# Kernel tuning notes

Measured on AMD Instinct MI355X. Metric: run time of the kernel, lower is better.

## Reference

```python
import jax, jax.numpy as jnp
import numpy as np

B, C, P, T = 16, 128, 512, 32
H = 2
D = C // H  # 64
SCALE = D ** -0.5  # note: original scales by d^-0.5, NOT (d*t)^-0.5


def setup_inputs() -> dict:
    key = jax.random.key(0)
    kx, kw, kb = jax.random.split(key, 3)
    x = jax.random.normal(kx, (B, C, P, T), dtype=jnp.float32)
    # Conv2d(C, 3C, kernel=1) == per-pixel linear: W:[3C, C], b:[3C]
    W = jax.random.normal(kw, (3 * C, C), dtype=jnp.float32) * (C ** -0.5)
    b = jax.random.normal(kb, (3 * C,), dtype=jnp.float32) * 0.01
    return {"x": x, "W": W, "b": b}


def reference(x, W, b):
    # 1x1 conv -> pointwise channel mix
    qkv = jnp.einsum('bcpt,oc->bopt', x, W) + b[None, :, None, None]  # [B,3C,P,T]
    qkv = qkv.reshape(B, 3, H, D, P, T)
    q, k, v = qkv[:, 0], qkv[:, 1], qkv[:, 2]  # each [B,H,D,P,T]
    # flatten (d t) as feature dim, tokens along P
    q = q.transpose(0, 1, 3, 2, 4).reshape(B, H, P, D * T)
    k = k.transpose(0, 1, 3, 2, 4).reshape(B, H, P, D * T)
    v = v.transpose(0, 1, 3, 2, 4).reshape(B, H, P, D * T)
    dots = jnp.einsum('bhpe,bhqe->bhpq', q, k) * SCALE  # [B,H,P,P]
    attn = jax.nn.softmax(dots, axis=-1)
    out = jnp.einsum('bhpq,bhqe->bhpe', attn, v)  # [B,H,P,D*T]
    # b h p (d t) -> b (h d) p t
    out = out.reshape(B, H, P, D, T).transpose(0, 1, 3, 2, 4).reshape(B, C, P, T)
    return out
```

## Files before the change

kernel.cpp:

```cpp
#include <hip/hip_runtime.h>

#define BB 16
#define CC 128
#define PP 512
#define TT 32
#define HH 2
#define DD 64
#define EE 2048
#define NPIX 16384
#define SCALE 0.125f

typedef _Float16 f16_t;
typedef _Float16 f16x8_t __attribute__((ext_vector_type(8)));
typedef _Float16 f16x4_t __attribute__((ext_vector_type(4)));
typedef float    f32x4_t __attribute__((ext_vector_type(4)));

#define AS_GLOBAL __attribute__((address_space(1)))
#define AS_LDS    __attribute__((address_space(3)))

__device__ __forceinline__ void async_ld16(const void* g, void* l) {
    __builtin_amdgcn_global_load_lds((const AS_GLOBAL void*)g,
                                     (AS_LDS void*)l, 16, 0, 0);
}

__device__ __forceinline__ void gemm_lds_bt(const f16_t* __restrict__ A, int lda,
                                            const f16_t* __restrict__ Bt, int ldb,
                                            int K, int m0, int n0,
                                            f16_t* As, f16_t* Bs,
                                            f32x4_t acc[4][4])
{
    const int tid  = threadIdx.x;
    const int lane = tid & 63;
    const int wave = tid >> 6;
    const int wm = wave & 1, wn = wave >> 1;
    const int quad = lane >> 4, l16 = lane & 15;

    const f16_t* gA0 = A  + (size_t)(m0 + lane)      * lda + wave * 8;
    const f16_t* gA1 = A  + (size_t)(m0 + 64 + lane) * lda + wave * 8;
    const f16_t* gB0 = Bt + (size_t)(n0 + lane)      * ldb + wave * 8;
    const f16_t* gB1 = Bt + (size_t)(n0 + 64 + lane) * ldb + wave * 8;
    f16_t* lA0 = As + (size_t)(wave * 128)      * 8;
    f16_t* lA1 = As + (size_t)(wave * 128 + 64) * 8;
    f16_t* lB0 = Bs + (size_t)(wave * 128)      * 8;
    f16_t* lB1 = Bs + (size_t)(wave * 128 + 64) * 8;

    const int ar = wm * 64 + l16;
    const int br = wn * 64 + l16;

    for (int k0 = 0; k0 < K; k0 += 32) {
        if (k0) __syncthreads();
        async_ld16(gA0 + k0, lA0);
        async_ld16(gA1 + k0, lA1);
        async_ld16(gB0 + k0, lB0);
        async_ld16(gB1 + k0, lB1);
        __syncthreads();

        f16x8_t af[4], bf[4];
#pragma unroll
        for (int mi = 0; mi < 4; ++mi)
            af[mi] = *(const f16x8_t*)(As + (size_t)(quad * 128 + ar + mi * 16) * 8);
#pragma unroll
        for (int ni = 0; ni < 4; ++ni)
            bf[ni] = *(const f16x8_t*)(Bs + (size_t)(quad * 128 + br + ni * 16) * 8);
#pragma unroll
        for (int mi = 0; mi < 4; ++mi)
#pragma unroll
            for (int ni = 0; ni < 4; ++ni)
                acc[mi][ni] = __builtin_amdgcn_mfma_f32_16x16x32_f16(
                    af[mi], bf[ni], acc[mi][ni], 0, 0, 0);
    }
}

__global__ __launch_bounds__(256) void wcvt_kernel(const float* __restrict__ W,
                                                   f16_t* __restrict__ Wh)
{
    const int i = (blockIdx.x * 256 + threadIdx.x) * 4;
    const float4 wv = *(const float4*)(W + i);
    f16x4_t t;
    t[0] = (_Float16)wv.x; t[1] = (_Float16)wv.y;
    t[2] = (_Float16)wv.z; t[3] = (_Float16)wv.w;
    *(f16x4_t*)(Wh + i) = t;
}

__global__ __launch_bounds__(256, 3) void proj_kernel(const float* __restrict__ x,
                                                      const f16_t* __restrict__ Wh,
                                                      const float* __restrict__ bias,
                                                      f16_t* __restrict__ q,
                                                      f16_t* __restrict__ k,
                                                      f16_t* __restrict__ v)
{
    __shared__ f16_t xs[CC * 128];
    __shared__ f16_t wbuf[8 * 128 * 8];
    const int b    = blockIdx.y;
    const int pt   = blockIdx.x;
    const int tid  = threadIdx.x;
    const int lane = tid & 63;
    const int wave = tid >> 6;
    const int wm   = wave & 1, wn = wave >> 1;
    const int quad = lane >> 4, l16 = lane & 15;
    const int pixb = pt * 128;

    const float* xb = x + (size_t)b * CC * NPIX;

#pragma unroll 2
    for (int r = 0; r < 8; ++r) {
        const int u  = r * 4 + wave;
        const int c0 = (u >> 1) * 8;
        const int pl = (u & 1) * 64 + lane;
        const float* g = xb + (size_t)c0 * NPIX + pixb + pl;
        float vv[8];
#pragma unroll
        for (int j = 0; j < 8; ++j) vv[j] = g[(size_t)j * NPIX];
        f16x8_t t;
#pragma unroll
        for (int j = 0; j < 8; ++j) t[j] = (_Float16)vv[j];
        *(f16x8_t*)((char*)xs + pl * 256 + ((c0 * 2) ^ ((pl & 15) << 4))) = t;
    }

    for (int s = 0; s < 3; ++s) {
        f32x4_t acc[4][4];
#pragma unroll
        for (int i = 0; i < 4; ++i)
#pragma unroll
            for (int j = 0; j < 4; ++j) acc[i][j] = (f32x4_t){0.f, 0.f, 0.f, 0.f};

#pragma unroll
        for (int khalf = 0; khalf < 2; ++khalf) {
            __syncthreads();
#pragma unroll
            for (int i = 0; i < 4; ++i) {
                const int idx = wave * 4 + i;
                const int ch  = idx >> 1;
                const int oh  = (idx & 1) * 64;
                async_ld16(Wh + (size_t)(s * 128 + oh + lane) * CC
                              + (khalf * 8 + ch) * 8,
                           wbuf + ((size_t)ch * 128 + oh) * 8);
            }
            __syncthreads();

#pragma unroll
            for (int kk = 0; kk < 2; ++kk) {
                const int k0  = khalf * 64 + kk * 32;
                const int kq  = k0 + quad * 8;
                const int chq = kk * 4 + quad;
                f16x8_t xf[4], wf[4];
#pragma unroll
                for (int mi = 0; mi < 4; ++mi) {
                    const int pl = wm * 64 + mi * 16 + l16;
                    xf[mi] = *(const f16x8_t*)((char*)xs + pl * 256 +
                                               ((kq * 2) ^ ((pl & 15) << 4)));
                }
#pragma unroll
                for (int ni = 0; ni < 4; ++ni) {
                    const int ol = wn * 64 + ni * 16 + l16;
                    wf[ni] = *(const f16x8_t*)(wbuf + ((size_t)chq * 128 + ol) * 8);
                }
#pragma unroll
                for (int mi = 0; mi < 4; ++mi)
#pragma unroll
                    for (int ni = 0; ni < 4; ++ni)
                        acc[mi][ni] = __builtin_amdgcn_mfma_f32_16x16x32_f16(
                            xf[mi], wf[ni], acc[mi][ni], 0, 0, 0);
            }
        }

        float bv[4];
#pragma unroll
        for (int ni = 0; ni < 4; ++ni)
            bv[ni] = bias[s * 128 + wn * 64 + ni * 16 + l16];

        f16_t* dst = (s == 0) ? q : (s == 1) ? k : v;
        const int h = wn;
#pragma unroll
        for (int mi = 0; mi < 4; ++mi) {
            const int pix0 = pixb + wm * 64 + mi * 16 + quad * 4;
            const int p  = pix0 >> 5;
            const int t0 = pix0 & 31;
#pragma unroll
            for (int ni = 0; ni < 4; ++ni) {
                const int d = ni * 16 + l16;
                f16x4_t o4;
#pragma unroll
                for (int r = 0; r < 4; ++r)
                    o4[r] = (_Float16)(acc[mi][ni][r] + bv[ni]);
                *(f16x4_t*)(dst + ((size_t)((b * HH + h) * PP + p)) * EE
                                + d * TT + t0) = o4;
            }
        }
    }
}

__global__ __launch_bounds__(256) void vpose_kernel(const f16_t* __restrict__ v,
                                                    f16_t* __restrict__ vt)
{
    __shared__ unsigned short lds[64][65];
    const int bh   = blockIdx.y;
    const int tile = blockIdx.x;
    const int e0 = (tile & 31) * 64;
    const int p0 = (tile >> 5) * 64;
    const int tid = threadIdx.x;
    const int rw  = tid >> 3;
    const int c8  = (tid & 7) * 8;
    const f16_t* vb  = v  + (size_t)bh * PP * EE;
    f16_t*       vtb = vt + (size_t)bh * EE * PP;
#pragma unroll
    for (int half = 0; half < 2; ++half) {
        const int p = rw + half * 32;
        const f16x8_t t = *(const f16x8_t*)(vb + (size_t)(p0 + p) * EE + e0 + c8);
#pragma unroll
        for (int j = 0; j < 8; ++j)
            lds[p][c8 + j] = __builtin_bit_cast(unsigned short, (_Float16)t[j]);
    }
    __syncthreads();
#pragma unroll
    for (int half = 0; half < 2; ++half) {
        const int e = rw + half * 32;
        f16x8_t t;
#pragma unroll
        for (int j = 0; j < 8; ++j)
            t[j] = __builtin_bit_cast(_Float16, lds[c8 + j][e]);
        *(f16x8_t*)(vtb + (size_t)(e0 + e) * PP + p0 + c8) = t;
    }
}

__global__ __launch_bounds__(256) void qk_kernel(const f16_t* __restrict__ q,
                                                 const f16_t* __restrict__ k,
                                                 float* __restrict__ S)
{
    __shared__ f16_t As[128 * 32];
    __shared__ f16_t Bs[128 * 32];
    const int id = blockIdx.x;
    const int bh = id & 31;
    const int tile = id >> 5;
    const int mt = tile & 3, nt = tile >> 2;
    const int tid  = threadIdx.x;
    const int lane = tid & 63;
    const int wave = tid >> 6;
    const int wm = wave & 1, wn = wave >> 1;
    const int quad = lane >> 4, l16 = lane & 15;

    f32x4_t acc[4][4];
#pragma unroll
    for (int i = 0; i < 4; ++i)
#pragma unroll
        for (int j = 0; j < 4; ++j) acc[i][j] = (f32x4_t){0.f, 0.f, 0.f, 0.f};

    const f16_t* qb = q + (size_t)bh * PP * EE;
    const f16_t* kb = k + (size_t)bh * PP * EE;
    gemm_lds_bt(qb, EE, kb, EE, EE, mt * 128, nt * 128, As, Bs, acc);

    float* Sb = S + (size_t)bh * PP * PP;
#pragma unroll
    for (int mi = 0; mi < 4; ++mi)
#pragma unroll
        for (int r = 0; r < 4; ++r) {
            const int row = mt * 128 + wm * 64 + mi * 16 + quad * 4 + r;
#pragma unroll
            for (int ni = 0; ni < 4; ++ni) {
                const int col = nt * 128 + wn * 64 + ni * 16 + l16;
                Sb[(size_t)row * PP + col] = acc[mi][ni][r] * SCALE;
            }
        }
}

__global__ __launch_bounds__(256) void softmax_kernel(float* __restrict__ S)
{
    const int tid  = threadIdx.x;
    const int wave = tid >> 6;
    const int lane = tid & 63;
    const int row  = blockIdx.x * 4 + wave;
    float* rp = S + (size_t)row * PP;

    const float4 a = *(const float4*)(rp + lane * 8);
    const float4 b = *(const float4*)(rp + lane * 8 + 4);

    float m = fmaxf(fmaxf(fmaxf(a.x, a.y), fmaxf(a.z, a.w)),
                    fmaxf(fmaxf(b.x, b.y), fmaxf(b.z, b.w)));
#pragma unroll
    for (int off = 1; off < 64; off <<= 1) m = fmaxf(m, __shfl_xor(m, off, 64));

    float e[8];
    e[0] = expf(a.x - m); e[1] = expf(a.y - m);
    e[2] = expf(a.z - m); e[3] = expf(a.w - m);
    e[4] = expf(b.x - m); e[5] = expf(b.y - m);
    e[6] = expf(b.z - m); e[7] = expf(b.w - m);

    float sum = e[0] + e[1] + e[2] + e[3] + e[4] + e[5] + e[6] + e[7];
#pragma unroll
    for (int off = 1; off < 64; off <<= 1) sum += __shfl_xor(sum, off, 64);
    const float inv = 1.0f / sum;

    __syncthreads();

    f16_t* prow = (f16_t*)rp;
    f16x8_t o;
#pragma unroll
    for (int j = 0; j < 8; ++j) o[j] = (_Float16)(e[j] * inv);
    *(f16x8_t*)(prow + lane * 8) = o;
}

__global__ __launch_bounds__(256) void pv_kernel(const f16_t* __restrict__ Pm,
                                                 const f16_t* __restrict__ vt,
                                                 float* __restrict__ out)
{
    __shared__ f16_t As[128 * 32];
    __shared__ f16_t Bs[128 * 32];
    const int id = blockIdx.x;
    const int bh = id & 31;
    const int tile = id >> 5;
    const int nt = tile & 3, mt = tile >> 2;
    const int tid  = threadIdx.x;
    const int lane = tid & 63;
    const int wave = tid >> 6;
    const int wm = wave & 1, wn = wave >> 1;
    const int quad = lane >> 4, l16 = lane & 15;

    f32x4_t acc[4][4];
#pragma unroll
    for (int i = 0; i < 4; ++i)
#pragma unroll
        for (int j = 0; j < 4; ++j) acc[i][j] = (f32x4_t){0.f, 0.f, 0.f, 0.f};

    const f16_t* Pb  = Pm + (size_t)bh * PP * 1024;
    const f16_t* vtb = vt + (size_t)bh * EE * PP;
    gemm_lds_bt(vtb, PP, Pb, 1024, PP, mt * 128, nt * 128, As, Bs, acc);

    const int b = bh >> 1, h = bh & 1;
#pragma unroll
    for (int mi = 0; mi < 4; ++mi) {
        const int e0 = mt * 128 + wm * 64 + mi * 16 + quad * 4;
        const int d  = e0 >> 5;
        const int t0 = e0 & 31;
#pragma unroll
        for (int ni = 0; ni < 4; ++ni) {
            const int p = nt * 128 + wn * 64 + ni * 16 + l16;
            *(f32x4_t*)(out + ((size_t)(b * CC + h * DD + d) * PP + p) * TT + t0)
                = acc[mi][ni];
        }
    }
}

extern "C" void kernel_launch(void* const* d_in, const int* in_sizes, int n_in,
                              void* d_out, int out_size, void* d_ws, size_t ws_size,
                              hipStream_t stream)
{
    const float* x    = (const float*)d_in[0];
    const float* W    = (const float*)d_in[1];
    const float* bias = (const float*)d_in[2];
    float* out = (float*)d_out;

    char* ws = (char*)d_ws;
    const size_t MiB = 1024ull * 1024ull;
    f16_t* q  = (f16_t*)(ws);
    f16_t* k  = (f16_t*)(ws + 64 * MiB);
    f16_t* v  = (f16_t*)(ws + 128 * MiB);
    f16_t* vt = (f16_t*)(ws + 192 * MiB);
    float* S  = (float*)(ws + 256 * MiB);
    f16_t* Wh = (f16_t*)(ws + 256 * MiB);

    wcvt_kernel<<<dim3(48), dim3(256), 0, stream>>>(W, Wh);
    proj_kernel<<<dim3(128, 16), dim3(256), 0, stream>>>(x, Wh, bias, q, k, v);
    vpose_kernel<<<dim3(256, 32), dim3(256), 0, stream>>>(v, vt);
    qk_kernel<<<dim3(512), dim3(256), 0, stream>>>(q, k, S);
    softmax_kernel<<<dim3(4096), dim3(256), 0, stream>>>(S);
    pv_kernel<<<dim3(2048), dim3(256), 0, stream>>>((const f16_t*)S, vt, out);
}
```

Before: 494.7 us.

## Double-buffer LDS tiles in QK and PV GEMMs to overlap loads with MFMA

Changes the shared GEMM loop so the next K-slice is loaded into a second LDS buffer with async global-to-LDS loads while MFMAs run on the current one. Explicit vmcnt waits and raw s_barrier calls replace the two __syncthreads per step. The goal is to hide global load latency in the QK and PV kernels. It doubles LDS per block to 32 KB, which can lower occupancy, and correctness depends on the hand-written waitcnt ordering.

```diff
diff --git a/kernel.cpp b/kernel.cpp
--- a/kernel.cpp
+++ b/kernel.cpp
@@ -23,51 +23,68 @@
                                      (AS_LDS void*)l, 16, 0, 0);
 }
 
-__device__ __forceinline__ void gemm_lds_bt(const f16_t* __restrict__ A, int lda,
-                                            const f16_t* __restrict__ Bt, int ldb,
-                                            int K, int m0, int n0,
-                                            f16_t* As, f16_t* Bs,
-                                            f32x4_t acc[4][4])
+__device__ __forceinline__ void gemm_lds_bt_pipe(const f16_t* __restrict__ A, int lda,
+                                                 const f16_t* __restrict__ Bt, int ldb,
+                                                 int K, int m0, int n0,
+                                                 f16_t* As, f16_t* Bs,
+                                                 f32x4_t acc[4][4])
 {
     const int tid  = threadIdx.x;
     const int lane = tid & 63;
     const int wave = tid >> 6;
     const int wm = wave & 1, wn = wave >> 1;
     const int quad = lane >> 4, l16 = lane & 15;
+    constexpr int TILE = 128 * 32;
 
     const f16_t* gA0 = A  + (size_t)(m0 + lane)      * lda + wave * 8;
     const f16_t* gA1 = A  + (size_t)(m0 + 64 + lane) * lda + wave * 8;
     const f16_t* gB0 = Bt + (size_t)(n0 + lane)      * ldb + wave * 8;
     const f16_t* gB1 = Bt + (size_t)(n0 + 64 + lane) * ldb + wave * 8;
-    f16_t* lA0 = As + (size_t)(wave * 128)      * 8;
-    f16_t* lA1 = As + (size_t)(wave * 128 + 64) * 8;
-    f16_t* lB0 = Bs + (size_t)(wave * 128)      * 8;
-    f16_t* lB1 = Bs + (size_t)(wave * 128 + 64) * 8;
 
     const int ar = wm * 64 + l16;
     const int br = wn * 64 + l16;
 
-    for (int k0 = 0; k0 < K; k0 += 32) {
-        if (k0) __syncthreads();
-        async_ld16(gA0 + k0, lA0);
-        async_ld16(gA1 + k0, lA1);
-        async_ld16(gB0 + k0, lB0);
-        async_ld16(gB1 + k0, lB1);
-        __syncthreads();
-
+    auto stage = [&](int buf, int k0) {
+        f16_t* dA = As + buf * TILE;
+        f16_t* dB = Bs + buf * TILE;
+        async_ld16(gA0 + k0, dA + (size_t)(wave * 128)      * 8);
+        async_ld16(gA1 + k0, dA + (size_t)(wave * 128 + 64) * 8);
+        async_ld16(gB0 + k0, dB + (size_t)(wave * 128)      * 8);
+        async_ld16(gB1 + k0, dB + (size_t)(wave * 128 + 64) * 8);
+    };
+
+    stage(0, 0);
+    int cur = 0;
+    const int nsteps = K >> 5;
+
+    for (int t = 0; t < nsteps; ++t) {
+        if (t + 1 < nsteps) {
+            stage(cur ^ 1, (t + 1) << 5);
+            asm volatile("s_waitcnt vmcnt(4)" ::: "memory");
+        } else {
+            asm volatile("s_waitcnt vmcnt(0)" ::: "memory");
+        }
+        __builtin_amdgcn_s_barrier();
+
+        const f16_t* sA = As + cur * TILE;
+        const f16_t* sB = Bs + cur * TILE;
         f16x8_t af[4], bf[4];
 #pragma unroll
         for (int mi = 0; mi < 4; ++mi)
-            af[mi] = *(const f16x8_t*)(As + (size_t)(quad * 128 + ar + mi * 16) * 8);
+            af[mi] = *(const f16x8_t*)(sA + (size_t)(quad * 128 + ar + mi * 16) * 8);
 #pragma unroll
         for (int ni = 0; ni < 4; ++ni)
-            bf[ni] = *(const f16x8_t*)(Bs + (size_t)(quad * 128 + br + ni * 16) * 8);
+            bf[ni] = *(const f16x8_t*)(sB + (size_t)(quad * 128 + br + ni * 16) * 8);
 #pragma unroll
         for (int mi = 0; mi < 4; ++mi)
 #pragma unroll
             for (int ni = 0; ni < 4; ++ni)
                 acc[mi][ni] = __builtin_amdgcn_mfma_f32_16x16x32_f16(
                     af[mi], bf[ni], acc[mi][ni], 0, 0, 0);
+
+        asm volatile("s_waitcnt lgkmcnt(0)" ::: "memory");
+        __builtin_amdgcn_s_barrier();
+        cur ^= 1;
     }
 }
 
@@ -227,8 +244,8 @@
                                                  const f16_t* __restrict__ k,
                                                  float* __restrict__ S)
 {
-    __shared__ f16_t As[128 * 32];
-    __shared__ f16_t Bs[128 * 32];
+    __shared__ f16_t As[2 * 128 * 32];
+    __shared__ f16_t Bs[2 * 128 * 32];
     const int id = blockIdx.x;
     const int bh = id & 31;
     const int tile = id >> 5;
@@ -247,7 +264,7 @@
 
     const f16_t* qb = q + (size_t)bh * PP * EE;
     const f16_t* kb = k + (size_t)bh * PP * EE;
-    gemm_lds_bt(qb, EE, kb, EE, EE, mt * 128, nt * 128, As, Bs, acc);
+    gemm_lds_bt_pipe(qb, EE, kb, EE, EE, mt * 128, nt * 128, As, Bs, acc);
 
     float* Sb = S + (size_t)bh * PP * PP;
 #pragma unroll
@@ -303,8 +320,8 @@
                                                  const f16_t* __restrict__ vt,
                                                  float* __restrict__ out)
 {
-    __shared__ f16_t As[128 * 32];
-    __shared__ f16_t Bs[128 * 32];
+    __shared__ f16_t As[2 * 128 * 32];
+    __shared__ f16_t Bs[2 * 128 * 32];
     const int id = blockIdx.x;
     const int bh = id & 31;
     const int tile = id >> 5;
@@ -323,7 +340,7 @@
 
     const f16_t* Pb  = Pm + (size_t)bh * PP * 1024;
     const f16_t* vtb = vt + (size_t)bh * EE * PP;
-    gemm_lds_bt(vtb, PP, Pb, 1024, PP, mt * 128, nt * 128, As, Bs, acc);
+    gemm_lds_bt_pipe(vtb, PP, Pb, 1024, PP, mt * 128, nt * 128, As, Bs, acc);
 
     const int b = bh >> 1, h = bh & 1;
 #pragma unroll
```

New measurement: 492.3 us. Within noise of the previous version (-0.5%).
